# Kernel tuning notes

Hardware: AMD Instinct MI355X
Metric: run time of the kernel (lower is better)

Reference implementation:

```python
import jax, jax.numpy as jnp
import numpy as np

B, S, D = 4, 2048, 1024
P = 2
N_FEAT = 16          # n_feature_know
N_REST = 16          # n_restore_know
R = 128              # knowledge_rank
D_SPACE = 64


def setup_inputs() -> dict:
    key = jax.random.key(0)
    ks = jax.random.split(key, 6)
    x = jax.random.normal(ks[0], (B, S, D), dtype=jnp.float32)
    # per-token routing weights for each of P feature paths, in [0,1)
    feature_paths = jax.random.uniform(ks[1], (P, B, S, N_FEAT), dtype=jnp.float32)
    f_know = jax.random.normal(ks[2], (N_FEAT, D, R), dtype=jnp.float32) * 0.02
    r_know = jax.random.normal(ks[3], (N_REST, R, D), dtype=jnp.float32) * 0.02
    feature_emb = jax.random.normal(ks[4], (N_FEAT, D_SPACE), dtype=jnp.float32)
    W_router = jax.random.normal(ks[5], (D_SPACE + R, N_REST), dtype=jnp.float32) * 0.05
    return {"x": x, "feature_paths": feature_paths, "f_know": f_know,
            "r_know": r_know, "feature_emb": feature_emb, "W_router": W_router}


def reference(x, feature_paths, f_know, r_know, feature_emb, W_router):
    # Feature projection into all N low-rank banks: [B,S,N,R]
    all_h = jnp.einsum('bsd,ndr->bsnr', x, f_know)
    # Weighted sum over banks per path: [P,B,S,R]
    h_all = jnp.einsum('bsnr,pbsn->pbsr', all_h, feature_paths)
    # Context for restore routing: [P,B,S,D_SPACE]
    neuron_ctx = jnp.einsum('pbsn,nd->pbsd', feature_paths, feature_emb)
    # restore_input = cat([neuron_ctx, h]) -> router -> softmax restore weights
    restore_input = jnp.concatenate([neuron_ctx, h_all], axis=-1)  # [P,B,S,D_SPACE+R]
    logits = jnp.einsum('pbsc,cn->pbsn', restore_input, W_router)
    w = jax.nn.softmax(logits, axis=-1)                            # [P,B,S,N_REST]
    # Restore + per-token weighted combine, summed over P paths: [B,S,D]
    output = jnp.einsum('pbsr,nrd,pbsn->bsd', h_all, r_know, w)
    restore_aux_loss = jnp.float32(0.0)
    return output, restore_aux_loss
```

## Files before the change

kernel.cpp:

```cpp
#include <hip/hip_runtime.h>

typedef __attribute__((ext_vector_type(4))) float f32x4;
typedef __bf16 bf16x8 __attribute__((ext_vector_type(8)));

#define T_TOK 8192
#define DIM   1024
#define NRCOL 2048

static __device__ __forceinline__ unsigned short f2bf(float f) {
  unsigned int u = __builtin_bit_cast(unsigned int, f);
  u += 0x7fffu + ((u >> 16) & 1u);
  return (unsigned short)(u >> 16);
}
static __device__ __forceinline__ float bfbits2f(unsigned int lo16) {
  return __builtin_bit_cast(float, lo16 << 16);
}
static __device__ __forceinline__ void gload16(const void* g, void* l) {
  __builtin_amdgcn_global_load_lds((const __attribute__((address_space(1))) void*)g,
                                   (__attribute__((address_space(3))) void*)l, 16, 0, 0);
}

__global__ __launch_bounds__(256) void cvt_f32_bf16(const float* __restrict__ in,
                                                    unsigned short* __restrict__ out,
                                                    int n4) {
  int i = blockIdx.x * 256 + threadIdx.x;
  const int stride = gridDim.x * 256;
  const float4* in4 = (const float4*)in;
  uint2* o4 = (uint2*)out;
  for (; i < n4; i += stride) {
    float4 v = in4[i];
    uint2 o;
    o.x = (unsigned)f2bf(v.x) | ((unsigned)f2bf(v.y) << 16);
    o.y = (unsigned)f2bf(v.z) | ((unsigned)f2bf(v.w) << 16);
    o4[i] = o;
  }
}

__global__ __launch_bounds__(256) void tcvt(const float* __restrict__ src,
                                            unsigned short* __restrict__ dst,
                                            int rows, int cols,
                                            long sstride, long dstride) {
  src += (size_t)blockIdx.z * sstride;
  dst += (size_t)blockIdx.z * dstride;
  __shared__ float tile[32][33];
  const int tx = threadIdx.x & 31, ty = threadIdx.x >> 5;
  const int r0 = blockIdx.y * 32, c0 = blockIdx.x * 32;
  #pragma unroll
  for (int i = 0; i < 32; i += 8)
    tile[ty + i][tx] = src[(size_t)(r0 + ty + i) * cols + c0 + tx];
  __syncthreads();
  #pragma unroll
  for (int i = 0; i < 32; i += 8)
    dst[(size_t)(c0 + ty + i) * rows + r0 + tx] = f2bf(tile[tx][ty + i]);
}

template<bool OUT_BF16>
__global__ __launch_bounds__(256) void gemm_bt(const unsigned short* __restrict__ A,
                                               const unsigned short* __restrict__ Bt,
                                               void* __restrict__ Cp,
                                               int M, int N, int K) {
  __shared__ unsigned short As[128 * 64];
  __shared__ unsigned short Bs[128 * 64];
  const int tid = threadIdx.x;
  const int bx = blockIdx.x, by = blockIdx.y;
  const int lane = tid & 63;
  const int wv = tid >> 6;
  const int wm = wv >> 1, wn = wv & 1;
  const int lrow = lane & 15;
  const int lk = lane >> 4;

  const unsigned short* Ab = A + (size_t)by * 128 * K;
  const unsigned short* Bb = Bt + (size_t)bx * 128 * K;

  f32x4 acc[4][4];
  #pragma unroll
  for (int m = 0; m < 4; ++m)
    #pragma unroll
    for (int n = 0; n < 4; ++n)
      acc[m][n] = (f32x4){0.f, 0.f, 0.f, 0.f};

  const int nk = K >> 6;
  for (int kt = 0; kt < nk; ++kt) {
    #pragma unroll
    for (int c = 0; c < 4; ++c) {
      const int L = c * 4096 + tid * 16;
      const int row = L >> 7;
      const int sc = ((L >> 4) & 7) ^ (row & 7);
      gload16(Ab + (size_t)row * K + kt * 64 + sc * 8, (void*)&As[L >> 1]);
      gload16(Bb + (size_t)row * K + kt * 64 + sc * 8, (void*)&Bs[L >> 1]);
    }
    __syncthreads();
    #pragma unroll
    for (int kk = 0; kk < 2; ++kk) {
      bf16x8 av[4], bv[4];
      #pragma unroll
      for (int m = 0; m < 4; ++m) {
        const int r = wm * 64 + m * 16 + lrow;
        const int ch = (kk * 4 + lk) ^ (r & 7);
        av[m] = *(const bf16x8*)&As[r * 64 + ch * 8];
      }
      #pragma unroll
      for (int n = 0; n < 4; ++n) {
        const int r = wn * 64 + n * 16 + lrow;
        const int ch = (kk * 4 + lk) ^ (r & 7);
        bv[n] = *(const bf16x8*)&Bs[r * 64 + ch * 8];
      }
      #pragma unroll
      for (int m = 0; m < 4; ++m)
        #pragma unroll
        for (int n = 0; n < 4; ++n)
          acc[m][n] = __builtin_amdgcn_mfma_f32_16x16x32_bf16(av[m], bv[n], acc[m][n], 0, 0, 0);
    }
    __syncthreads();
  }

  #pragma unroll
  for (int m = 0; m < 4; ++m) {
    const int row0 = by * 128 + wm * 64 + m * 16 + lk * 4;
    #pragma unroll
    for (int n = 0; n < 4; ++n) {
      const int col = bx * 128 + wn * 64 + n * 16 + lrow;
      #pragma unroll
      for (int j = 0; j < 4; ++j) {
        const size_t idx = (size_t)(row0 + j) * N + col;
        if (OUT_BF16) ((unsigned short*)Cp)[idx] = f2bf(acc[m][n][j]);
        else          ((float*)Cp)[idx] = acc[m][n][j];
      }
    }
  }
}

__global__ __launch_bounds__(256) void middle_kernel(const unsigned short* __restrict__ AH,
                                                     const float* __restrict__ fp,
                                                     const float* __restrict__ femb,
                                                     const float* __restrict__ Wr,
                                                     unsigned short* __restrict__ Mout,
                                                     float* __restrict__ auxout) {
  __shared__ float G[16][16];
  __shared__ float hs[4][2][128];
  __shared__ float wsm[4][2][16];
  const int tid = threadIdx.x;
  {
    const int n = tid >> 4, j = tid & 15;
    float s = 0.f;
    #pragma unroll
    for (int ds = 0; ds < 64; ++ds) s += femb[n * 64 + ds] * Wr[ds * 16 + j];
    G[n][j] = s;
  }
  const int wv = tid >> 6, l = tid & 63;
  const int t = blockIdx.x * 4 + wv;

  float p0[16], p1[16];
  #pragma unroll
  for (int n = 0; n < 16; ++n) {
    p0[n] = fp[t * 16 + n];
    p1[n] = fp[T_TOK * 16 + t * 16 + n];
  }

  float h00 = 0.f, h01 = 0.f, h10 = 0.f, h11 = 0.f;
  const unsigned short* ahrow = AH + (size_t)t * NRCOL;
  #pragma unroll
  for (int n = 0; n < 16; ++n) {
    const unsigned int v = *(const unsigned int*)(ahrow + n * 128 + 2 * l);
    const float a0 = bfbits2f(v & 0xffffu);
    const float a1 = bfbits2f(v >> 16);
    h00 += a0 * p0[n]; h01 += a1 * p0[n];
    h10 += a0 * p1[n]; h11 += a1 * p1[n];
  }
  hs[wv][0][2 * l] = h00; hs[wv][0][2 * l + 1] = h01;
  hs[wv][1][2 * l] = h10; hs[wv][1][2 * l + 1] = h11;
  __syncthreads();

  if (l < 32) {
    const int p = l >> 4, j = l & 15;
    float s = 0.f;
    #pragma unroll
    for (int n = 0; n < 16; ++n) s += (p ? p1[n] : p0[n]) * G[n][j];
    for (int r = 0; r < 128; ++r) s += hs[wv][p][r] * Wr[(64 + r) * 16 + j];
    float mx = s;
    #pragma unroll
    for (int d = 1; d < 16; d <<= 1) mx = fmaxf(mx, __shfl_xor(mx, d, 64));
    const float e = __expf(s - mx);
    float sum = e;
    #pragma unroll
    for (int d = 1; d < 16; d <<= 1) sum += __shfl_xor(sum, d, 64);
    wsm[wv][p][j] = e / sum;
  }
  __syncthreads();

  unsigned short* mrow = Mout + (size_t)t * NRCOL;
  #pragma unroll
  for (int n = 0; n < 16; ++n) {
    const float w0 = wsm[wv][0][n], w1 = wsm[wv][1][n];
    const float m0 = w0 * h00 + w1 * h10;
    const float m1 = w0 * h01 + w1 * h11;
    const unsigned int pk = (unsigned)f2bf(m0) | ((unsigned)f2bf(m1) << 16);
    *(unsigned int*)(mrow + n * 128 + 2 * l) = pk;
  }
  if (blockIdx.x == 0 && tid == 0) auxout[0] = 0.f;
}

extern "C" void kernel_launch(void* const* d_in, const int* in_sizes, int n_in,
                              void* d_out, int out_size, void* d_ws, size_t ws_size,
                              hipStream_t stream) {
  const float* x    = (const float*)d_in[0];
  const float* fp   = (const float*)d_in[1];
  const float* fk   = (const float*)d_in[2];
  const float* rk   = (const float*)d_in[3];
  const float* femb = (const float*)d_in[4];
  const float* Wr   = (const float*)d_in[5];
  float* out = (float*)d_out;

  char* ws = (char*)d_ws;
  unsigned short* Xbf = (unsigned short*)ws;
  unsigned short* W1t = (unsigned short*)(ws + 16u * 1024 * 1024);
  unsigned short* Mb  = (unsigned short*)ws;
  unsigned short* W2t = (unsigned short*)(ws + 32u * 1024 * 1024);
  unsigned short* AH  = (unsigned short*)(ws + 36u * 1024 * 1024);

  cvt_f32_bf16<<<2048, 256, 0, stream>>>(x, Xbf, (T_TOK * DIM) / 4);
  tcvt<<<dim3(128 / 32, 1024 / 32, 16), 256, 0, stream>>>(fk, W1t, 1024, 128,
                                                          1024L * 128, 128L * 1024);
  tcvt<<<dim3(1024 / 32, 2048 / 32, 1), 256, 0, stream>>>(rk, W2t, 2048, 1024, 0, 0);
  gemm_bt<true><<<dim3(NRCOL / 128, T_TOK / 128), 256, 0, stream>>>(Xbf, W1t, AH,
                                                                    T_TOK, NRCOL, DIM);
  middle_kernel<<<T_TOK / 4, 256, 0, stream>>>(AH, fp, femb, Wr, Mb, out + 8388608);
  gemm_bt<false><<<dim3(DIM / 128, T_TOK / 128), 256, 0, stream>>>(Mb, W2t, out,
                                                                   T_TOK, DIM, NRCOL);
}
```

Baseline: 133.0 us.

## Replace GEMMs with 8-wave double-buffered 256-row tiles and block swizzle

```diff
diff --git a/kernel.cpp b/kernel.cpp
--- a/kernel.cpp
+++ b/kernel.cpp
@@ -2,10 +2,16 @@
 
 typedef __attribute__((ext_vector_type(4))) float f32x4;
 typedef __bf16 bf16x8 __attribute__((ext_vector_type(8)));
+typedef unsigned short ushort_t;
 
 #define T_TOK 8192
 #define DIM   1024
 #define NRCOL 2048
+
+#define LGKM0() asm volatile("s_waitcnt lgkmcnt(0)" ::: "memory")
+#define VMW(n)  asm volatile("s_waitcnt vmcnt(" #n ")" ::: "memory")
+#define SB0()   __builtin_amdgcn_sched_barrier(0)
+#define BAR()   __builtin_amdgcn_s_barrier()
 
 static __device__ __forceinline__ unsigned short f2bf(float f) {
   unsigned int u = __builtin_bit_cast(unsigned int, f);
@@ -54,77 +60,113 @@
     dst[(size_t)(c0 + ty + i) * rows + r0 + tx] = f2bf(tile[tx][ty + i]);
 }
 
-template<bool OUT_BF16>
-__global__ __launch_bounds__(256) void gemm_bt(const unsigned short* __restrict__ A,
-                                               const unsigned short* __restrict__ Bt,
-                                               void* __restrict__ Cp,
-                                               int M, int N, int K) {
-  __shared__ unsigned short As[128 * 64];
-  __shared__ unsigned short Bs[128 * 64];
+template<int BN, bool OUT_BF16>
+__global__ __launch_bounds__(512) void gemm8(const ushort_t* __restrict__ A,
+                                             const ushort_t* __restrict__ Bt,
+                                             void* __restrict__ Cp,
+                                             int N, int K) {
+  constexpr int NF = BN / 64;
+  constexpr int BR = BN / 64;
+  constexpr int LPT = 4 + BR;
+  __shared__ ushort_t As[2][256 * 64];
+  __shared__ ushort_t Bs[2][BN * 64];
+
   const int tid = threadIdx.x;
-  const int bx = blockIdx.x, by = blockIdx.y;
-  const int lane = tid & 63;
-  const int wv = tid >> 6;
-  const int wm = wv >> 1, wn = wv & 1;
-  const int lrow = lane & 15;
-  const int lk = lane >> 4;
-
-  const unsigned short* Ab = A + (size_t)by * 128 * K;
-  const unsigned short* Bb = Bt + (size_t)bx * 128 * K;
-
-  f32x4 acc[4][4];
-  #pragma unroll
-  for (int m = 0; m < 4; ++m)
-    #pragma unroll
-    for (int n = 0; n < 4; ++n)
+  const int nx = gridDim.x;
+  const int orig = blockIdx.y * nx + blockIdx.x;
+  const int q = (nx * gridDim.y) >> 3;
+  const int swz = (orig & 7) * q + (orig >> 3);
+  const int bx = swz % nx, by = swz / nx;
+
+  const int lane = tid & 63, wv = tid >> 6;
+  const int wm = wv >> 2, wn = wv & 3;
+  const int lrow = lane & 15, lk = lane >> 4;
+
+  const ushort_t* Ab = A + (size_t)by * 256 * K;
+  const ushort_t* Bb = Bt + (size_t)bx * BN * K;
+
+  auto stage = [&](int c, int kt) {
+    #pragma unroll
+    for (int r = 0; r < 4; ++r) {
+      const int off = r * 8192 + tid * 16;
+      const int row = off >> 7;
+      const int ch = ((off >> 4) & 7) ^ (row & 7);
+      gload16(Ab + (size_t)row * K + kt * 64 + ch * 8, (void*)&As[c][off >> 1]);
+    }
+    #pragma unroll
+    for (int r = 0; r < BR; ++r) {
+      const int off = r * 8192 + tid * 16;
+      const int row = off >> 7;
+      const int ch = ((off >> 4) & 7) ^ (row & 7);
+      gload16(Bb + (size_t)row * K + kt * 64 + ch * 8, (void*)&Bs[c][off >> 1]);
+    }
+  };
+
+  f32x4 acc[8][NF];
+  #pragma unroll
+  for (int m = 0; m < 8; ++m)
+    #pragma unroll
+    for (int n = 0; n < NF; ++n)
       acc[m][n] = (f32x4){0.f, 0.f, 0.f, 0.f};
 
-  const int nk = K >> 6;
-  for (int kt = 0; kt < nk; ++kt) {
-    #pragma unroll
-    for (int c = 0; c < 4; ++c) {
-      const int L = c * 4096 + tid * 16;
-      const int row = L >> 7;
-      const int sc = ((L >> 4) & 7) ^ (row & 7);
-      gload16(Ab + (size_t)row * K + kt * 64 + sc * 8, (void*)&As[L >> 1]);
-      gload16(Bb + (size_t)row * K + kt * 64 + sc * 8, (void*)&Bs[L >> 1]);
-    }
-    __syncthreads();
-    #pragma unroll
-    for (int kk = 0; kk < 2; ++kk) {
-      bf16x8 av[4], bv[4];
-      #pragma unroll
-      for (int m = 0; m < 4; ++m) {
-        const int r = wm * 64 + m * 16 + lrow;
-        const int ch = (kk * 4 + lk) ^ (r & 7);
-        av[m] = *(const bf16x8*)&As[r * 64 + ch * 8];
+  const int nt = K >> 6;
+  stage(0, 0);
+  stage(1, 1);
+  if constexpr (LPT == 8) VMW(8); else VMW(6);
+  SB0(); BAR(); SB0();
+
+  for (int t = 0; t < nt; ++t) {
+    const int c = t & 1;
+    bf16x8 av[8][2], bv[NF][2];
+    #pragma unroll
+    for (int m = 0; m < 8; ++m)
+      #pragma unroll
+      for (int ks = 0; ks < 2; ++ks) {
+        const int row = wm * 128 + m * 16 + lrow;
+        const int ch = (ks * 4 + lk) ^ (row & 7);
+        av[m][ks] = *(const bf16x8*)&As[c][row * 64 + ch * 8];
       }
-      #pragma unroll
-      for (int n = 0; n < 4; ++n) {
-        const int r = wn * 64 + n * 16 + lrow;
-        const int ch = (kk * 4 + lk) ^ (r & 7);
-        bv[n] = *(const bf16x8*)&Bs[r * 64 + ch * 8];
+    #pragma unroll
+    for (int n = 0; n < NF; ++n)
+      #pragma unroll
+      for (int ks = 0; ks < 2; ++ks) {
+        const int row = wn * (BN / 4) + n * 16 + lrow;
+        const int ch = (ks * 4 + lk) ^ (row & 7);
+        bv[n][ks] = *(const bf16x8*)&Bs[c][row * 64 + ch * 8];
       }
-      #pragma unroll
-      for (int m = 0; m < 4; ++m)
+    LGKM0();
+    SB0();
+    BAR();
+    SB0();
+    if (t + 2 < nt) stage(c, t + 2);
+    __builtin_amdgcn_s_setprio(1);
+    #pragma unroll
+    for (int ks = 0; ks < 2; ++ks)
+      #pragma unroll
+      for (int m = 0; m < 8; ++m)
         #pragma unroll
-        for (int n = 0; n < 4; ++n)
-          acc[m][n] = __builtin_amdgcn_mfma_f32_16x16x32_bf16(av[m], bv[n], acc[m][n], 0, 0, 0);
-    }
-    __syncthreads();
-  }
-
-  #pragma unroll
-  for (int m = 0; m < 4; ++m) {
-    const int row0 = by * 128 + wm * 64 + m * 16 + lk * 4;
-    #pragma unroll
-    for (int n = 0; n < 4; ++n) {
-      const int col = bx * 128 + wn * 64 + n * 16 + lrow;
+        for (int n = 0; n < NF; ++n)
+          acc[m][n] = __builtin_amdgcn_mfma_f32_16x16x32_bf16(av[m][ks], bv[n][ks], acc[m][n], 0, 0, 0);
+    __builtin_amdgcn_s_setprio(0);
+    SB0();
+    if (t + 2 < nt) { if constexpr (LPT == 8) VMW(8); else VMW(6); }
+    else if (t + 1 < nt) VMW(0);
+    SB0();
+    BAR();
+    SB0();
+  }
+
+  #pragma unroll
+  for (int m = 0; m < 8; ++m) {
+    const int row0 = by * 256 + wm * 128 + m * 16 + lk * 4;
+    #pragma unroll
+    for (int n = 0; n < NF; ++n) {
+      const int col = bx * BN + wn * (BN / 4) + n * 16 + lrow;
       #pragma unroll
       for (int j = 0; j < 4; ++j) {
         const size_t idx = (size_t)(row0 + j) * N + col;
-        if (OUT_BF16) ((unsigned short*)Cp)[idx] = f2bf(acc[m][n][j]);
-        else          ((float*)Cp)[idx] = acc[m][n][j];
+        if constexpr (OUT_BF16) ((ushort_t*)Cp)[idx] = f2bf(acc[m][n][j]);
+        else                    ((float*)Cp)[idx] = acc[m][n][j];
       }
     }
   }
@@ -222,9 +264,9 @@
   tcvt<<<dim3(128 / 32, 1024 / 32, 16), 256, 0, stream>>>(fk, W1t, 1024, 128,
                                                           1024L * 128, 128L * 1024);
   tcvt<<<dim3(1024 / 32, 2048 / 32, 1), 256, 0, stream>>>(rk, W2t, 2048, 1024, 0, 0);
-  gemm_bt<true><<<dim3(NRCOL / 128, T_TOK / 128), 256, 0, stream>>>(Xbf, W1t, AH,
-                                                                    T_TOK, NRCOL, DIM);
+  gemm8<256, true><<<dim3(NRCOL / 256, T_TOK / 256), 512, 0, stream>>>(Xbf, W1t, AH,
+                                                                       NRCOL, DIM);
   middle_kernel<<<T_TOK / 4, 256, 0, stream>>>(AH, fp, femb, Wr, Mb, out + 8388608);
-  gemm_bt<false><<<dim3(DIM / 128, T_TOK / 128), 256, 0, stream>>>(Mb, W2t, out,
-                                                                   T_TOK, DIM, NRCOL);
-}
+  gemm8<128, false><<<dim3(DIM / 128, T_TOK / 256), 512, 0, stream>>>(Mb, W2t, out,
+                                                                      DIM, NRCOL);
+}
```

After: 120.0 us. -9.8%, faster.
